# Performance work log

Measured on AMD Instinct MI355X. Metric: run time of the kernel, lower is better.

The kernel has to match this reference:

```python
import jax, jax.numpy as jnp
import numpy as np

DIM = 2048; HEADS = 16; KV_HEADS = 8; HEAD_DIM = 128; RANK = 16; INNER = 5632
B = 2; S = 2048; EPS = 1e-5


def setup_inputs() -> dict:
    key = jax.random.key(0)
    ks = jax.random.split(key, 32)
    r = lambda i, shape, scale=0.02: jax.random.normal(ks[i], shape, jnp.float32) * scale
    theta = jax.random.uniform(ks[0], (S, HEAD_DIM // 2), jnp.float32, 0.0, 2.0 * np.pi)
    return {
        "hidden_states": jax.random.normal(ks[1], (B, S, DIM), jnp.float32),
        "attention_mask": jnp.ones((B, S), jnp.bool_),
        "rope_cos": jnp.cos(theta),
        "rope_sin": jnp.sin(theta),
        "wq_a": r(2, (DIM, RANK), 1.0), "wq_b": r(3, (RANK, DIM)), "bq": r(4, (DIM,)),
        "wk_a": r(5, (DIM, RANK), 1.0), "wk_b": r(6, (RANK, KV_HEADS * HEAD_DIM)), "bk": r(7, (KV_HEADS * HEAD_DIM,)),
        "wv_a": r(8, (DIM, RANK), 1.0), "wv_b": r(9, (RANK, KV_HEADS * HEAD_DIM)), "bv": r(10, (KV_HEADS * HEAD_DIM,)),
        "norm_q_w": 1.0 + r(11, (DIM,)), "norm_q_b": r(12, (DIM,)),
        "norm_k_w": 1.0 + r(13, (KV_HEADS * HEAD_DIM,)), "norm_k_b": r(14, (KV_HEADS * HEAD_DIM,)),
        "w1_a": r(15, (DIM, RANK), 1.0), "w1_b": r(16, (RANK, INNER)), "b1": r(17, (INNER,)),
        "w3_a": r(18, (DIM, RANK), 1.0), "w3_b": r(19, (RANK, INNER)), "b3": r(20, (INNER,)),
        "w2_a": r(21, (INNER, RANK), 1.0), "w2_b": r(22, (RANK, DIM)), "b2": r(23, (DIM,)),
        "norm_w": 1.0 + r(24, (DIM,)), "ffn_norm_w": 1.0 + r(25, (DIM,)),
    }


def _rms(x, w):
    return x * jax.lax.rsqrt(jnp.mean(x * x, axis=-1, keepdims=True) + EPS) * w


def _ln(x, w, b):
    m = jnp.mean(x, axis=-1, keepdims=True)
    v = jnp.mean((x - m) ** 2, axis=-1, keepdims=True)
    return (x - m) * jax.lax.rsqrt(v + EPS) * w + b


def _lora(x, wa, wb, b):
    # faithful to x @ (WA@WB)/rank + b, computed as chained low-rank matmuls
    return (x @ wa) @ wb * (1.0 / RANK) + b


def _rope(x, cos, sin):
    # x: [B,S,H,D]; interleaved-pair complex rotation (diffusers use_real=False)
    x0, x1 = x[..., 0::2], x[..., 1::2]
    c = cos[None, :, None, :]
    s = sin[None, :, None, :]
    return jnp.stack([x0 * c - x1 * s, x0 * s + x1 * c], axis=-1).reshape(x.shape)


def reference(hidden_states, attention_mask, rope_cos, rope_sin,
              wq_a, wq_b, bq, wk_a, wk_b, bk, wv_a, wv_b, bv,
              norm_q_w, norm_q_b, norm_k_w, norm_k_b,
              w1_a, w1_b, b1, w3_a, w3_b, b3, w2_a, w2_b, b2,
              norm_w, ffn_norm_w):
    B_, S_, D_ = hidden_states.shape
    residual = hidden_states
    nh = _rms(hidden_states, norm_w)
    # QKV via LoRA linears; QK layer-norm across heads (before head split)
    q = _ln(_lora(nh, wq_a, wq_b, bq), norm_q_w, norm_q_b)
    k = _ln(_lora(nh, wk_a, wk_b, bk), norm_k_w, norm_k_b)
    v = _lora(nh, wv_a, wv_b, bv)
    q = _rope(q.reshape(B_, S_, HEADS, HEAD_DIM), rope_cos, rope_sin)
    k = _rope(k.reshape(B_, S_, KV_HEADS, HEAD_DIM), rope_cos, rope_sin)
    v = v.reshape(B_, S_, KV_HEADS, HEAD_DIM)
    # GQA: repeat each kv head n_rep times consecutively
    n_rep = HEADS // KV_HEADS
    k = jnp.repeat(k, n_rep, axis=2)
    v = jnp.repeat(v, n_rep, axis=2)
    scale = 1.0 / np.sqrt(HEAD_DIM).astype(np.float32)
    scores = jnp.einsum('bqhd,bkhd->bhqk', q, k) * scale
    neg = jnp.asarray(jnp.finfo(scores.dtype).min, scores.dtype)
    scores = jnp.where(attention_mask[:, None, None, :], scores, neg)
    attn = jax.nn.softmax(scores, axis=-1)
    attn_out = jnp.einsum('bhqk,bkhd->bqhd', attn, v).reshape(B_, S_, D_)
    h = residual + attn_out  # processor output flattened; no to_out in this block
    nf = _rms(h, ffn_norm_w)
    mlp = _lora(jax.nn.silu(_lora(nf, w1_a, w1_b, b1)) * _lora(nf, w3_a, w3_b, b3), w2_a, w2_b, b2)
    return h + mlp
```

## Files before the change

### kernel.cpp

```cpp
#include <hip/hip_runtime.h>
#include <math.h>

typedef unsigned short u16;
typedef unsigned int u32;
typedef __bf16 bf16x8 __attribute__((ext_vector_type(8)));
typedef __bf16 bf16x4 __attribute__((ext_vector_type(4)));
typedef float f32x4 __attribute__((ext_vector_type(4)));

#define DIM 2048
#define NHEADS 16
#define NKVH 8
#define HD 128
#define RANK 16
#define INNER 5632
#define BB 2
#define SS 2048
#define NROWS (BB*SS)
#define EPS 1e-5f
#define QSC2 0.12751743560829201f
#define LOG2E 1.4426950408889634f

__device__ inline float bf2f(u16 u){ u32 x = ((u32)u)<<16; float f; __builtin_memcpy(&f,&x,4); return f; }
__device__ inline u16 f2bf(float f){ u32 u; __builtin_memcpy(&u,&f,4); u32 r = u + 0x7fffu + ((u>>16)&1u); return (u16)(r>>16); }
__device__ inline u32 pack2(float a, float b){ return (u32)f2bf(a) | ((u32)f2bf(b)<<16); }
__device__ inline u16 bfu(float f){ __bf16 b = (__bf16)f; u16 r; __builtin_memcpy(&r,&b,2); return r; }

__device__ inline float blockReduceSum(float v){
  __shared__ float r[4];
  #pragma unroll
  for(int o=1;o<64;o<<=1) v += __shfl_xor(v, o);
  int wv = threadIdx.x>>6;
  __syncthreads();
  if((threadIdx.x&63)==0) r[wv] = v;
  __syncthreads();
  return r[0]+r[1]+r[2]+r[3];
}

__device__ inline f32x4 blockReduceSum4(f32x4 v){
  __shared__ f32x4 r4[4];
  #pragma unroll
  for(int o=1;o<64;o<<=1){
    v.x += __shfl_xor(v.x,o); v.y += __shfl_xor(v.y,o);
    v.z += __shfl_xor(v.z,o); v.w += __shfl_xor(v.w,o);
  }
  int wv = threadIdx.x>>6;
  __syncthreads();
  if((threadIdx.x&63)==0) r4[wv]=v;
  __syncthreads();
  return r4[0]+r4[1]+r4[2]+r4[3];
}

__global__ __launch_bounds__(256) void k_castw(const float* __restrict__ wqb,
                                               const float* __restrict__ wkb,
                                               const float* __restrict__ wvb,
                                               const float* __restrict__ w2b,
                                               u16* __restrict__ wqP,
                                               u16* __restrict__ wkvP,
                                               u16* __restrict__ w2P){
  int bid = blockIdx.x;
  const float* src; u16* dst; int off;
  if(bid<16){ src=wqb; dst=wqP; off=bid; }
  else if(bid<24){ src=wkb; dst=wkvP; off=bid-16; }
  else if(bid<32){ src=wvb; dst=wkvP+16384; off=bid-24; }
  else { src=w2b; dst=w2P; off=bid-32; }
  int base = off*2048 + threadIdx.x*8;
  float4 a = ((const float4*)src)[base/4];
  float4 c = ((const float4*)src)[base/4+1];
  uint4 st;
  st.x = pack2(a.x,a.y); st.y = pack2(a.z,a.w);
  st.z = pack2(c.x,c.y); st.w = pack2(c.z,c.w);
  *(uint4*)&dst[base] = st;
}

__global__ __launch_bounds__(256) void k_rms(const float* __restrict__ x,
                                             const float* __restrict__ w,
                                             u16* __restrict__ out){
  size_t base = (size_t)blockIdx.x*DIM;
  int tid = threadIdx.x;
  float4 v0 = ((const float4*)(x+base))[tid*2];
  float4 v1 = ((const float4*)(x+base))[tid*2+1];
  float ss = v0.x*v0.x+v0.y*v0.y+v0.z*v0.z+v0.w*v0.w
           + v1.x*v1.x+v1.y*v1.y+v1.z*v1.z+v1.w*v1.w;
  ss = blockReduceSum(ss);
  float rstd = rsqrtf(ss*(1.0f/DIM) + EPS);
  float4 w0 = ((const float4*)w)[tid*2];
  float4 w1 = ((const float4*)w)[tid*2+1];
  uint4 st;
  st.x = pack2(v0.x*w0.x*rstd, v0.y*w0.y*rstd);
  st.y = pack2(v0.z*w0.z*rstd, v0.w*w0.w*rstd);
  st.z = pack2(v1.x*w1.x*rstd, v1.y*w1.y*rstd);
  st.w = pack2(v1.z*w1.z*rstd, v1.w*w1.w*rstd);
  *(uint4*)&out[base + tid*8] = st;
}

template<int NMAT>
__global__ __launch_bounds__(256) void k_loraAm(const u16* __restrict__ X,
                                                const float* __restrict__ A0,
                                                const float* __restrict__ A1,
                                                const float* __restrict__ A2,
                                                float* __restrict__ out){
  constexpr int LDO = NMAT*16;
  int mat = blockIdx.x >> 6;
  int blk = blockIdx.x & 63;
  const float* A = (mat==0) ? A0 : ((NMAT>2 && mat==2) ? A2 : A1);
  int tid = threadIdx.x;
  int ks = tid&15, rg = tid>>4;
  int row0 = blk*64 + rg*4;
  float acc[4][16];
  #pragma unroll
  for(int r=0;r<4;r++)
    #pragma unroll
    for(int c=0;c<16;c++) acc[r][c]=0.f;
  const u16* xp = X + (size_t)row0*DIM + ks*128;
  for(int i8=0;i8<16;i8++){
    bf16x8 x0 = *(const bf16x8*)(xp + i8*8);
    bf16x8 x1 = *(const bf16x8*)(xp + DIM + i8*8);
    bf16x8 x2 = *(const bf16x8*)(xp + 2*DIM + i8*8);
    bf16x8 x3 = *(const bf16x8*)(xp + 3*DIM + i8*8);
    #pragma unroll
    for(int e=0;e<8;e++){
      const float4* a = (const float4*)(A + ((size_t)(ks*128 + i8*8 + e))*16);
      float4 a0=a[0], a1=a[1], a2=a[2], a3=a[3];
      float xs0=(float)x0[e], xs1=(float)x1[e], xs2=(float)x2[e], xs3=(float)x3[e];
      #define FMAROW(r, xs) \
        acc[r][0]=fmaf(xs,a0.x,acc[r][0]); acc[r][1]=fmaf(xs,a0.y,acc[r][1]); \
        acc[r][2]=fmaf(xs,a0.z,acc[r][2]); acc[r][3]=fmaf(xs,a0.w,acc[r][3]); \
        acc[r][4]=fmaf(xs,a1.x,acc[r][4]); acc[r][5]=fmaf(xs,a1.y,acc[r][5]); \
        acc[r][6]=fmaf(xs,a1.z,acc[r][6]); acc[r][7]=fmaf(xs,a1.w,acc[r][7]); \
        acc[r][8]=fmaf(xs,a2.x,acc[r][8]); acc[r][9]=fmaf(xs,a2.y,acc[r][9]); \
        acc[r][10]=fmaf(xs,a2.z,acc[r][10]); acc[r][11]=fmaf(xs,a2.w,acc[r][11]); \
        acc[r][12]=fmaf(xs,a3.x,acc[r][12]); acc[r][13]=fmaf(xs,a3.y,acc[r][13]); \
        acc[r][14]=fmaf(xs,a3.z,acc[r][14]); acc[r][15]=fmaf(xs,a3.w,acc[r][15]);
      FMAROW(0, xs0) FMAROW(1, xs1) FMAROW(2, xs2) FMAROW(3, xs3)
      #undef FMAROW
    }
  }
  #pragma unroll
  for(int o=1;o<16;o<<=1){
    #pragma unroll
    for(int r=0;r<4;r++)
      #pragma unroll
      for(int c=0;c<16;c++) acc[r][c] += __shfl_xor(acc[r][c], o);
  }
  if(ks==0){
    #pragma unroll
    for(int r=0;r<4;r++){
      float4* op = (float4*)(out + (size_t)(row0+r)*LDO + mat*16);
      op[0] = make_float4(acc[r][0],acc[r][1],acc[r][2],acc[r][3]);
      op[1] = make_float4(acc[r][4],acc[r][5],acc[r][6],acc[r][7]);
      op[2] = make_float4(acc[r][8],acc[r][9],acc[r][10],acc[r][11]);
      op[3] = make_float4(acc[r][12],acc[r][13],acc[r][14],acc[r][15]);
    }
  }
}

__global__ __launch_bounds__(256) void k_qb(const float* __restrict__ xa,
                                            const u16* __restrict__ wqP,
                                            const float* __restrict__ bq,
                                            const float* __restrict__ nqw,
                                            const float* __restrict__ nqb,
                                            const float* __restrict__ cosT,
                                            const float* __restrict__ sinT,
                                            u16* __restrict__ qout){
  __shared__ u16 wl[16*2048];
  int tid = threadIdx.x;
  #pragma unroll
  for(int ii=0;ii<16;ii++)
    ((uint4*)wl)[tid + 256*ii] = ((const uint4*)wqP)[tid + 256*ii];
  __syncthreads();
  int j0 = tid*8;
  float bqv[8], nwv[8], nbv[8];
  #pragma unroll
  for(int e=0;e<8;e++){ bqv[e]=bq[j0+e]; nwv[e]=nqw[j0+e]; nbv[e]=nqb[j0+e]; }
  int i0 = (j0&127)>>1;
  for(int rp=0;rp<4;rp++){
    int row = blockIdx.x*8 + rp*2;
    float pre[2][8];
    #pragma unroll
    for(int rr=0;rr<2;rr++){
      float xq[16];
      #pragma unroll
      for(int r=0;r<16;r++) xq[r] = xa[(size_t)(row+rr)*48 + r];
      #pragma unroll
      for(int e=0;e<8;e++) pre[rr][e]=0.f;
      #pragma unroll
      for(int r=0;r<16;r++){
        bf16x8 wv = *(const bf16x8*)&wl[r*2048 + j0];
        #pragma unroll
        for(int e=0;e<8;e++) pre[rr][e] = fmaf(xq[r], (float)wv[e], pre[rr][e]);
      }
      #pragma unroll
      for(int e=0;e<8;e++) pre[rr][e] = pre[rr][e]*0.0625f + bqv[e];
    }
    f32x4 sv = (f32x4){0.f,0.f,0.f,0.f};
    #pragma unroll
    for(int e=0;e<8;e++){
      sv.x += pre[0][e]; sv.y += pre[0][e]*pre[0][e];
      sv.z += pre[1][e]; sv.w += pre[1][e]*pre[1][e];
    }
    f32x4 red = blockReduceSum4(sv);
    #pragma unroll
    for(int rr=0;rr<2;rr++){
      float mu  = (rr?red.z:red.x)*(1.0f/DIM);
      float var = (rr?red.w:red.y)*(1.0f/DIM) - mu*mu;
      float rstd = rsqrtf(var + EPS);
      float qn[8];
      #pragma unroll
      for(int e=0;e<8;e++) qn[e] = (pre[rr][e]-mu)*rstd*nwv[e] + nbv[e];
      int spos = (row+rr) & (SS-1);
      const float* cp = cosT + spos*64;
      const float* sp = sinT + spos*64;
      uint4 st;
      u32 pk[4];
      #pragma unroll
      for(int p=0;p<4;p++){
        float c = cp[i0+p], sn = sp[i0+p];
        float x0 = qn[2*p], x1 = qn[2*p+1];
        pk[p] = pack2((x0*c - x1*sn)*QSC2, (x0*sn + x1*c)*QSC2);
      }
      st.x=pk[0]; st.y=pk[1]; st.z=pk[2]; st.w=pk[3];
      *(uint4*)&qout[(size_t)(row+rr)*2048 + j0] = st;
    }
  }
}

__global__ __launch_bounds__(256) void k_kvb(const float* __restrict__ xa,
                                             const u16* __restrict__ wkvP,
                                             const float* __restrict__ bk,
                                             const float* __restrict__ nkw,
                                             const float* __restrict__ nkb,
                                             const float* __restrict__ bv,
                                             const float* __restrict__ cosT,
                                             const float* __restrict__ sinT,
                                             u16* __restrict__ kout,
                                             u16* __restrict__ vout){
  __shared__ u16 wl[2*16*1024];
  int tid = threadIdx.x;
  #pragma unroll
  for(int ii=0;ii<16;ii++)
    ((uint4*)wl)[tid + 256*ii] = ((const uint4*)wkvP)[tid + 256*ii];
  __syncthreads();
  int j0 = tid*4;
  float bkv[4], nwv[4], nbv[4], bvv[4];
  #pragma unroll
  for(int e=0;e<4;e++){ bkv[e]=bk[j0+e]; nwv[e]=nkw[j0+e]; nbv[e]=nkb[j0+e]; bvv[e]=bv[j0+e]; }
  int i0 = (j0&127)>>1;
  for(int rp=0;rp<4;rp++){
    int row = blockIdx.x*8 + rp*2;
    float pk_[2][4], pv_[2][4];
    #pragma unroll
    for(int rr=0;rr<2;rr++){
      float xk[16], xv[16];
      #pragma unroll
      for(int r=0;r<16;r++){ xk[r]=xa[(size_t)(row+rr)*48+16+r]; xv[r]=xa[(size_t)(row+rr)*48+32+r]; }
      #pragma unroll
      for(int e=0;e<4;e++){ pk_[rr][e]=0.f; pv_[rr][e]=0.f; }
      #pragma unroll
      for(int r=0;r<16;r++){
        bf16x4 wk4 = *(const bf16x4*)&wl[r*1024 + j0];
        bf16x4 wv4 = *(const bf16x4*)&wl[16384 + r*1024 + j0];
        #pragma unroll
        for(int e=0;e<4;e++){ pk_[rr][e]=fmaf(xk[r],(float)wk4[e],pk_[rr][e]); pv_[rr][e]=fmaf(xv[r],(float)wv4[e],pv_[rr][e]); }
      }
      #pragma unroll
      for(int e=0;e<4;e++){ pk_[rr][e]=pk_[rr][e]*0.0625f + bkv[e]; pv_[rr][e]=pv_[rr][e]*0.0625f + bvv[e]; }
    }
    f32x4 sv = (f32x4){0.f,0.f,0.f,0.f};
    #pragma unroll
    for(int e=0;e<4;e++){
      sv.x += pk_[0][e]; sv.y += pk_[0][e]*pk_[0][e];
      sv.z += pk_[1][e]; sv.w += pk_[1][e]*pk_[1][e];
    }
    f32x4 red = blockReduceSum4(sv);
    #pragma unroll
    for(int rr=0;rr<2;rr++){
      float mu  = (rr?red.z:red.x)*(1.0f/1024.0f);
      float var = (rr?red.w:red.y)*(1.0f/1024.0f) - mu*mu;
      float rstd = rsqrtf(var + EPS);
      float kn[4];
      #pragma unroll
      for(int e=0;e<4;e++) kn[e] = (pk_[rr][e]-mu)*rstd*nwv[e] + nbv[e];
      int spos = (row+rr) & (SS-1);
      const float* cp = cosT + spos*64;
      const float* sp = sinT + spos*64;
      uint2 stk;
      { float c=cp[i0],   sn=sp[i0];   stk.x = pack2(kn[0]*c - kn[1]*sn, kn[0]*sn + kn[1]*c); }
      { float c=cp[i0+1], sn=sp[i0+1]; stk.y = pack2(kn[2]*c - kn[3]*sn, kn[2]*sn + kn[3]*c); }
      *(uint2*)&kout[(size_t)(row+rr)*1024 + j0] = stk;
      uint2 stv; stv.x = pack2(pv_[rr][0],pv_[rr][1]); stv.y = pack2(pv_[rr][2],pv_[rr][3]);
      *(uint2*)&vout[(size_t)(row+rr)*1024 + j0] = stv;
    }
  }
}

__global__ __launch_bounds__(256) void k_vt(const u16* __restrict__ v,
                                            u16* __restrict__ vt){
  __shared__ u16 tl[64*68];
  int bid = blockIdx.x;
  int st = bid & 31;
  int dt = (bid>>5) & 1;
  int bh = bid>>6;
  int b = bh>>3, kvh = bh&7;
  int tid = threadIdx.x;
  int s0 = st*64, d0 = dt*64;
  {
    int s_l = tid>>2, dg = tid&3;
    const u16* src = v + ((size_t)(b*SS + s0 + s_l)*NKVH + kvh)*HD + d0 + dg*16;
    *(uint4*)&tl[s_l*68 + dg*16]     = *(const uint4*)(src);
    *(uint4*)&tl[s_l*68 + dg*16 + 8] = *(const uint4*)(src + 8);
  }
  __syncthreads();
  {
    int d_l = tid>>2, sg = tid&3;
    u32 pk[8];
    #pragma unroll
    for(int i=0;i<8;i++){
      u16 a = tl[(sg*16 + 2*i)*68 + d_l];
      u16 c = tl[(sg*16 + 2*i+1)*68 + d_l];
      pk[i] = (u32)a | ((u32)c<<16);
    }
    u16* dst = vt + ((size_t)bh*HD + d0 + d_l)*SS + s0 + sg*16;
    ((uint4*)dst)[0] = make_uint4(pk[0],pk[1],pk[2],pk[3]);
    ((uint4*)dst)[1] = make_uint4(pk[4],pk[5],pk[6],pk[7]);
  }
}

__global__ __launch_bounds__(256,2) void k_attn(const u16* __restrict__ qb,
                                                const u16* __restrict__ kb,
                                                const u16* __restrict__ vt,
                                                const float* __restrict__ resid,
                                                float* __restrict__ out){
  __shared__ u16 Kc[16*520];
  __shared__ u16 Vc[8*1032];
  __shared__ u16 Pl[4][32*72];
  int bid = ((int)blockIdx.x & 7)*64 + ((int)blockIdx.x >> 3);
  int qt = bid & 15;
  int h  = (bid>>4) & 15;
  int b  = bid>>8;
  int kvh = h>>1;
  int tid = threadIdx.x;
  int w = tid>>6, lane = tid&63;
  int l16 = lane&15, lg = lane>>4;

  bf16x8 qa[2][4];
  #pragma unroll
  for(int m=0;m<2;m++){
    const u16* qp = qb + ((size_t)(b*SS + qt*128 + w*32 + m*16 + l16))*DIM + h*HD + lg*8;
    #pragma unroll
    for(int c=0;c<4;c++) qa[m][c] = *(const bf16x8*)(qp + c*32);
  }
  f32x4 acc[2][8];
  #pragma unroll
  for(int m=0;m<2;m++)
    #pragma unroll
    for(int n=0;n<8;n++) acc[m][n] = (f32x4){0.f,0.f,0.f,0.f};
  f32x4 lacc0 = (f32x4){0.f,0.f,0.f,0.f};
  f32x4 lacc1 = (f32x4){0.f,0.f,0.f,0.f};
  bf16x8 ones;
  #pragma unroll
  for(int e=0;e<8;e++) ones[e] = (__bf16)1.0f;

  u16* Pw = Pl[w];
  const u16* vtb = vt + (size_t)(b*NKVH + kvh)*HD*SS;
  const u16* kbb = kb + ((size_t)(b*SS)*NKVH + kvh)*HD;
  int k_key = tid>>4, k_dg = tid&15;
  int v_d   = tid>>3, v_kc = tid&7;
  uint4 kA,kB,kC,kD,vA,vB,vC,vD;

#define LOAD_STAGE(KT) do{ \
    const u16* ksrc_ = kbb + (size_t)(KT)*64*1024; \
    const u16* vsrc_ = vtb + (KT)*64; \
    kA = *(const uint4*)(ksrc_ + (size_t)(k_key     )*1024 + k_dg*8); \
    kB = *(const uint4*)(ksrc_ + (size_t)(k_key + 16)*1024 + k_dg*8); \
    kC = *(const uint4*)(ksrc_ + (size_t)(k_key + 32)*1024 + k_dg*8); \
    kD = *(const uint4*)(ksrc_ + (size_t)(k_key + 48)*1024 + k_dg*8); \
    vA = *(const uint4*)(vsrc_ + (size_t)(v_d      )*SS + v_kc*8); \
    vB = *(const uint4*)(vsrc_ + (size_t)(v_d + 32 )*SS + v_kc*8); \
    vC = *(const uint4*)(vsrc_ + (size_t)(v_d + 64 )*SS + v_kc*8); \
    vD = *(const uint4*)(vsrc_ + (size_t)(v_d + 96 )*SS + v_kc*8); \
  }while(0)
#define STORE_STAGE() do{ \
    *(uint4*)&Kc[k_dg*520 + (k_key     )*8] = kA; \
    *(uint4*)&Kc[k_dg*520 + (k_key + 16)*8] = kB; \
    *(uint4*)&Kc[k_dg*520 + (k_key + 32)*8] = kC; \
    *(uint4*)&Kc[k_dg*520 + (k_key + 48)*8] = kD; \
    *(uint4*)&Vc[v_kc*1032 + (v_d      )*8] = vA; \
    *(uint4*)&Vc[v_kc*1032 + (v_d + 32 )*8] = vB; \
    *(uint4*)&Vc[v_kc*1032 + (v_d + 64 )*8] = vC; \
    *(uint4*)&Vc[v_kc*1032 + (v_d + 96 )*8] = vD; \
  }while(0)

  LOAD_STAGE(0);
  STORE_STAGE();
  __syncthreads();

  for(int kt=0; kt<SS/64; kt++){
    bool more = (kt+1) < SS/64;
    if(more) LOAD_STAGE(kt+1);
    #pragma unroll
    for(int nb=0;nb<4;nb++){
      f32x4 s0 = (f32x4){0.f,0.f,0.f,0.f};
      f32x4 s1 = (f32x4){0.f,0.f,0.f,0.f};
      #pragma unroll
      for(int c=0;c<4;c++){
        bf16x8 kf = *(const bf16x8*)&Kc[(c*4+lg)*520 + (nb*16+l16)*8];
        s0 = __builtin_amdgcn_mfma_f32_16x16x32_bf16(qa[0][c], kf, s0, 0,0,0);
        s1 = __builtin_amdgcn_mfma_f32_16x16x32_bf16(qa[1][c], kf, s1, 0,0,0);
      }
      #pragma unroll
      for(int r=0;r<4;r++){
        Pw[(lg*4+r)*72 + nb*16 + l16]      = bfu(exp2f(s0[r]));
        Pw[(16+lg*4+r)*72 + nb*16 + l16]   = bfu(exp2f(s1[r]));
      }
    }
    #pragma unroll
    for(int ks=0;ks<2;ks++){
      bf16x8 pa0 = *(const bf16x8*)&Pw[l16*72 + ks*32 + lg*8];
      bf16x8 pa1 = *(const bf16x8*)&Pw[(16+l16)*72 + ks*32 + lg*8];
      lacc0 = __builtin_amdgcn_mfma_f32_16x16x32_bf16(pa0, ones, lacc0, 0,0,0);
      lacc1 = __builtin_amdgcn_mfma_f32_16x16x32_bf16(pa1, ones, lacc1, 0,0,0);
      #pragma unroll
      for(int n=0;n<8;n++){
        bf16x8 vf = *(const bf16x8*)&Vc[(ks*4+lg)*1032 + (n*16+l16)*8];
        acc[0][n] = __builtin_amdgcn_mfma_f32_16x16x32_bf16(pa0, vf, acc[0][n], 0,0,0);
        acc[1][n] = __builtin_amdgcn_mfma_f32_16x16x32_bf16(pa1, vf, acc[1][n], 0,0,0);
      }
    }
    __syncthreads();
    if(more) STORE_STAGE();
    __syncthreads();
  }
#undef LOAD_STAGE
#undef STORE_STAGE
  #pragma unroll
  for(int m=0;m<2;m++){
    #pragma unroll
    for(int r=0;r<4;r++){
      float lv = m ? lacc1[r] : lacc0[r];
      float inv = __builtin_amdgcn_rcpf(lv);
      int row = qt*128 + w*32 + m*16 + lg*4 + r;
      size_t base = ((size_t)(b*SS + row))*DIM + h*HD;
      #pragma unroll
      for(int n=0;n<8;n++){
        int d = n*16 + l16;
        out[base + d] = resid[base + d] + acc[m][n][r]*inv;
      }
    }
  }
}

__global__ __launch_bounds__(256) void k_pack(const float* __restrict__ w1b,
                                              const float* __restrict__ w3b,
                                              const float* __restrict__ w2a,
                                              u16* __restrict__ wpk){
  int j = blockIdx.x*256 + threadIdx.x;
  u32 pw[24];
  #pragma unroll
  for(int i=0;i<8;i++) pw[i]    = pack2(w1b[(size_t)(2*i)*INNER+j], w1b[(size_t)(2*i+1)*INNER+j]);
  #pragma unroll
  for(int i=0;i<8;i++) pw[8+i]  = pack2(w3b[(size_t)(2*i)*INNER+j], w3b[(size_t)(2*i+1)*INNER+j]);
  const float4* wp = (const float4*)(w2a + (size_t)j*16);
  #pragma unroll
  for(int q=0;q<4;q++){ float4 t=wp[q];
    pw[16+2*q] = pack2(t.x,t.y); pw[17+2*q] = pack2(t.z,t.w); }
  uint4* dst = (uint4*)(wpk + (size_t)j*48);
  #pragma unroll
  for(int i=0;i<6;i++) dst[i] = make_uint4(pw[4*i],pw[4*i+1],pw[4*i+2],pw[4*i+3]);
}

__global__ __launch_bounds__(256,1) void k_ffn(const float* __restrict__ t13,
                                               const u16* __restrict__ wpk,
                                               const float* __restrict__ b1,
                                               const float* __restrict__ b3,
                                               float* __restrict__ racc){
  __shared__ float tl[4][32];
  __shared__ float red[4][64];
  int tid = threadIdx.x;
  int row0 = blockIdx.x*4;
  if(tid<128) tl[tid>>5][tid&31] = t13[(size_t)row0*32 + tid];
  __syncthreads();
  float acc[64];
  #pragma unroll
  for(int v=0;v<64;v++) acc[v]=0.f;
  for(int ii=0;ii<INNER/256;ii++){
    int j = tid + 256*ii;
    const u16* wr = wpk + (size_t)j*48;
    bf16x8 W1a = *(const bf16x8*)(wr),    bf16x8_W1b_ = *(const bf16x8*)(wr+8);
    bf16x8 W1b = bf16x8_W1b_;
    bf16x8 W3a = *(const bf16x8*)(wr+16), W3b = *(const bf16x8*)(wr+24);
    bf16x8 W2a = *(const bf16x8*)(wr+32), W2b = *(const bf16x8*)(wr+40);
    float bb1 = b1[j], bb3 = b3[j];
    #pragma unroll
    for(int rr=0;rr<4;rr++){
      float a1=0.f, a3=0.f;
      #pragma unroll
      for(int r=0;r<8;r++){
        a1 = fmaf(tl[rr][r],    (float)W1a[r], a1);
        a1 = fmaf(tl[rr][8+r],  (float)W1b[r], a1);
        a3 = fmaf(tl[rr][16+r], (float)W3a[r], a3);
        a3 = fmaf(tl[rr][24+r], (float)W3b[r], a3);
      }
      a1 = a1*0.0625f + bb1;
      a3 = a3*0.0625f + bb3;
      float u = a1*__builtin_amdgcn_rcpf(1.0f+exp2f(-a1*LOG2E)) * a3;
      #pragma unroll
      for(int c=0;c<8;c++){
        acc[rr*16+c]   = fmaf(u, (float)W2a[c], acc[rr*16+c]);
        acc[rr*16+8+c] = fmaf(u, (float)W2b[c], acc[rr*16+8+c]);
      }
    }
  }
  #pragma unroll
  for(int o=1;o<64;o<<=1){
    #pragma unroll
    for(int v=0;v<64;v++) acc[v] += __shfl_xor(acc[v], o);
  }
  int wv = tid>>6, lane = tid&63;
  if(lane==0){
    #pragma unroll
    for(int v=0;v<64;v++) red[wv][v] = acc[v];
  }
  __syncthreads();
  if(tid<64){
    float sum = red[0][tid]+red[1][tid]+red[2][tid]+red[3][tid];
    racc[(size_t)(row0 + (tid>>4))*16 + (tid&15)] = sum;
  }
}

__global__ __launch_bounds__(256) void k_out(const float* __restrict__ racc,
                                             const u16* __restrict__ w2P,
                                             const float* __restrict__ b2,
                                             float* __restrict__ io){
  __shared__ u16 wl[16*2048];
  int tid = threadIdx.x;
  #pragma unroll
  for(int ii=0;ii<16;ii++)
    ((uint4*)wl)[tid + 256*ii] = ((const uint4*)w2P)[tid + 256*ii];
  __syncthreads();
  int j0 = tid*8;
  float b2v[8];
  #pragma unroll
  for(int e=0;e<8;e++) b2v[e] = b2[j0+e];
  for(int rr=0;rr<8;rr++){
    int row = blockIdx.x*8 + rr;
    float rc[16];
    #pragma unroll
    for(int r=0;r<16;r++) rc[r] = racc[(size_t)row*16 + r];
    float pre[8];
    #pragma unroll
    for(int e=0;e<8;e++) pre[e]=0.f;
    #pragma unroll
    for(int r=0;r<16;r++){
      bf16x8 wv = *(const bf16x8*)&wl[r*2048 + j0];
      #pragma unroll
      for(int e=0;e<8;e++) pre[e] = fmaf(rc[r], (float)wv[e], pre[e]);
    }
    float* op = io + (size_t)row*DIM + j0;
    float4 h0 = ((const float4*)op)[0];
    float4 h1 = ((const float4*)op)[1];
    float4 o0, o1;
    o0.x = h0.x + pre[0]*0.0625f + b2v[0];
    o0.y = h0.y + pre[1]*0.0625f + b2v[1];
    o0.z = h0.z + pre[2]*0.0625f + b2v[2];
    o0.w = h0.w + pre[3]*0.0625f + b2v[3];
    o1.x = h1.x + pre[4]*0.0625f + b2v[4];
    o1.y = h1.y + pre[5]*0.0625f + b2v[5];
    o1.z = h1.z + pre[6]*0.0625f + b2v[6];
    o1.w = h1.w + pre[7]*0.0625f + b2v[7];
    ((float4*)op)[0] = o0;
    ((float4*)op)[1] = o1;
  }
}

extern "C" void kernel_launch(void* const* d_in, const int* in_sizes, int n_in,
                              void* d_out, int out_size, void* d_ws, size_t ws_size,
                              hipStream_t stream){
  const float* hidden = (const float*)d_in[0];
  const float* cosT = (const float*)d_in[2];
  const float* sinT = (const float*)d_in[3];
  const float* wq_a = (const float*)d_in[4];
  const float* wq_b = (const float*)d_in[5];
  const float* bq   = (const float*)d_in[6];
  const float* wk_a = (const float*)d_in[7];
  const float* wk_b = (const float*)d_in[8];
  const float* bk   = (const float*)d_in[9];
  const float* wv_a = (const float*)d_in[10];
  const float* wv_b = (const float*)d_in[11];
  const float* bv   = (const float*)d_in[12];
  const float* nqw  = (const float*)d_in[13];
  const float* nqb  = (const float*)d_in[14];
  const float* nkw  = (const float*)d_in[15];
  const float* nkb  = (const float*)d_in[16];
  const float* w1a  = (const float*)d_in[17];
  const float* w1b  = (const float*)d_in[18];
  const float* b1   = (const float*)d_in[19];
  const float* w3a  = (const float*)d_in[20];
  const float* w3b  = (const float*)d_in[21];
  const float* b3   = (const float*)d_in[22];
  const float* w2a  = (const float*)d_in[23];
  const float* w2b  = (const float*)d_in[24];
  const float* b2   = (const float*)d_in[25];
  const float* normw  = (const float*)d_in[26];
  const float* fnormw = (const float*)d_in[27];
  float* out = (float*)d_out;

  char* p = (char*)d_ws;
  u16* bufA = (u16*)p; p += (size_t)NROWS*DIM*2;
  u16* qbuf = (u16*)p; p += (size_t)NROWS*DIM*2;
  u16* kbuf = (u16*)p; p += (size_t)NROWS*1024*2;
  u16* vbuf = (u16*)p; p += (size_t)NROWS*1024*2;
  float* xa   = (float*)p; p += (size_t)NROWS*48*4;
  float* t13  = (float*)p; p += (size_t)NROWS*32*4;
  float* racc = (float*)p; p += (size_t)NROWS*16*4;
  u16* wpk  = (u16*)p; p += (size_t)INNER*48*2;
  u16* wqP  = (u16*)p; p += (size_t)16*2048*2;
  u16* wkvP = (u16*)p; p += (size_t)2*16*1024*2;
  u16* w2P  = (u16*)p; p += (size_t)16*2048*2;
  u16* vtbuf = bufA;

  k_castw<<<48,256,0,stream>>>(wq_b, wk_b, wv_b, w2b, wqP, wkvP, w2P);
  k_pack<<<INNER/256,256,0,stream>>>(w1b, w3b, w2a, wpk);
  k_rms<<<NROWS,256,0,stream>>>(hidden, normw, bufA);
  k_loraAm<3><<<192,256,0,stream>>>(bufA, wq_a, wk_a, wv_a, xa);
  k_qb <<<NROWS/8,256,0,stream>>>(xa, wqP, bq, nqw, nqb, cosT, sinT, qbuf);
  k_kvb<<<NROWS/8,256,0,stream>>>(xa, wkvP, bk, nkw, nkb, bv, cosT, sinT, kbuf, vbuf);
  k_vt<<<1024,256,0,stream>>>(vbuf, vtbuf);
  k_attn<<<512,256,0,stream>>>(qbuf, kbuf, vtbuf, hidden, out);
  k_rms<<<NROWS,256,0,stream>>>(out, fnormw, bufA);
  k_loraAm<2><<<128,256,0,stream>>>(bufA, w1a, w3a, nullptr, t13);
  k_ffn<<<NROWS/4,256,0,stream>>>(t13, wpk, b1, b3, racc);
  k_out<<<NROWS/8,256,0,stream>>>(racc, w2P, b2, out);
}
```

Before: 389.9 us.

## Fuse RMSNorm into the LoRA-A projection, reading fp32 activations directly

Removes the separate RMSNorm kernels and the bf16 normalized intermediate buffer. Each row's sum of squares is now computed inside the LoRA-A kernel by a 16-lane shuffle reduction, and the fp32 input is normalized on the fly. Rows per block drop from 64 to 16 (one row per 16-thread group) and the grid grows. In exchange, each fp32 row is read twice and once per A matrix, so 3x or 2x redundant activation reads, and register reuse of the A weights across rows is lost.

Result: slower. 568.3 us (+45.7%).

```diff
diff --git a/kernel.cpp b/kernel.cpp
--- a/kernel.cpp
+++ b/kernel.cpp
@@ -24,17 +24,6 @@
 __device__ inline u16 f2bf(float f){ u32 u; __builtin_memcpy(&u,&f,4); u32 r = u + 0x7fffu + ((u>>16)&1u); return (u16)(r>>16); }
 __device__ inline u32 pack2(float a, float b){ return (u32)f2bf(a) | ((u32)f2bf(b)<<16); }
 __device__ inline u16 bfu(float f){ __bf16 b = (__bf16)f; u16 r; __builtin_memcpy(&r,&b,2); return r; }
-
-__device__ inline float blockReduceSum(float v){
-  __shared__ float r[4];
-  #pragma unroll
-  for(int o=1;o<64;o<<=1) v += __shfl_xor(v, o);
-  int wv = threadIdx.x>>6;
-  __syncthreads();
-  if((threadIdx.x&63)==0) r[wv] = v;
-  __syncthreads();
-  return r[0]+r[1]+r[2]+r[3];
-}
 
 __device__ inline f32x4 blockReduceSum4(f32x4 v){
   __shared__ f32x4 r4[4];
@@ -72,85 +61,66 @@
   *(uint4*)&dst[base] = st;
 }
 
-__global__ __launch_bounds__(256) void k_rms(const float* __restrict__ x,
-                                             const float* __restrict__ w,
-                                             u16* __restrict__ out){
-  size_t base = (size_t)blockIdx.x*DIM;
-  int tid = threadIdx.x;
-  float4 v0 = ((const float4*)(x+base))[tid*2];
-  float4 v1 = ((const float4*)(x+base))[tid*2+1];
-  float ss = v0.x*v0.x+v0.y*v0.y+v0.z*v0.z+v0.w*v0.w
-           + v1.x*v1.x+v1.y*v1.y+v1.z*v1.z+v1.w*v1.w;
-  ss = blockReduceSum(ss);
-  float rstd = rsqrtf(ss*(1.0f/DIM) + EPS);
-  float4 w0 = ((const float4*)w)[tid*2];
-  float4 w1 = ((const float4*)w)[tid*2+1];
-  uint4 st;
-  st.x = pack2(v0.x*w0.x*rstd, v0.y*w0.y*rstd);
-  st.y = pack2(v0.z*w0.z*rstd, v0.w*w0.w*rstd);
-  st.z = pack2(v1.x*w1.x*rstd, v1.y*w1.y*rstd);
-  st.w = pack2(v1.z*w1.z*rstd, v1.w*w1.w*rstd);
-  *(uint4*)&out[base + tid*8] = st;
-}
-
 template<int NMAT>
-__global__ __launch_bounds__(256) void k_loraAm(const u16* __restrict__ X,
-                                                const float* __restrict__ A0,
-                                                const float* __restrict__ A1,
-                                                const float* __restrict__ A2,
-                                                float* __restrict__ out){
+__global__ __launch_bounds__(256) void k_loraF(const float* __restrict__ X,
+                                               const float* __restrict__ nw,
+                                               const float* __restrict__ A0,
+                                               const float* __restrict__ A1,
+                                               const float* __restrict__ A2,
+                                               float* __restrict__ out){
   constexpr int LDO = NMAT*16;
-  int mat = blockIdx.x >> 6;
-  int blk = blockIdx.x & 63;
+  int mat = blockIdx.x >> 8;
+  int blk = blockIdx.x & 255;
   const float* A = (mat==0) ? A0 : ((NMAT>2 && mat==2) ? A2 : A1);
   int tid = threadIdx.x;
   int ks = tid&15, rg = tid>>4;
-  int row0 = blk*64 + rg*4;
-  float acc[4][16];
-  #pragma unroll
-  for(int r=0;r<4;r++)
-    #pragma unroll
-    for(int c=0;c<16;c++) acc[r][c]=0.f;
-  const u16* xp = X + (size_t)row0*DIM + ks*128;
-  for(int i8=0;i8<16;i8++){
-    bf16x8 x0 = *(const bf16x8*)(xp + i8*8);
-    bf16x8 x1 = *(const bf16x8*)(xp + DIM + i8*8);
-    bf16x8 x2 = *(const bf16x8*)(xp + 2*DIM + i8*8);
-    bf16x8 x3 = *(const bf16x8*)(xp + 3*DIM + i8*8);
-    #pragma unroll
-    for(int e=0;e<8;e++){
-      const float4* a = (const float4*)(A + ((size_t)(ks*128 + i8*8 + e))*16);
+  int row = blk*16 + rg;
+  const float* xp = X + (size_t)row*DIM + ks*128;
+  const float* wp = nw + ks*128;
+  float ss = 0.f;
+  #pragma unroll
+  for(int i=0;i<32;i++){
+    float4 v = ((const float4*)xp)[i];
+    ss += v.x*v.x + v.y*v.y + v.z*v.z + v.w*v.w;
+  }
+  ss += __shfl_xor(ss,1); ss += __shfl_xor(ss,2);
+  ss += __shfl_xor(ss,4); ss += __shfl_xor(ss,8);
+  float rstd = rsqrtf(ss*(1.0f/DIM) + EPS);
+  float acc[16];
+  #pragma unroll
+  for(int c=0;c<16;c++) acc[c]=0.f;
+  for(int i4=0;i4<32;i4++){
+    float4 xv = ((const float4*)xp)[i4];
+    float4 wv = ((const float4*)wp)[i4];
+    float xn[4];
+    xn[0]=xv.x*wv.x*rstd; xn[1]=xv.y*wv.y*rstd;
+    xn[2]=xv.z*wv.z*rstd; xn[3]=xv.w*wv.w*rstd;
+    #pragma unroll
+    for(int j=0;j<4;j++){
+      const float4* a = (const float4*)(A + ((size_t)(ks*128 + i4*4 + j))*16);
       float4 a0=a[0], a1=a[1], a2=a[2], a3=a[3];
-      float xs0=(float)x0[e], xs1=(float)x1[e], xs2=(float)x2[e], xs3=(float)x3[e];
-      #define FMAROW(r, xs) \
-        acc[r][0]=fmaf(xs,a0.x,acc[r][0]); acc[r][1]=fmaf(xs,a0.y,acc[r][1]); \
-        acc[r][2]=fmaf(xs,a0.z,acc[r][2]); acc[r][3]=fmaf(xs,a0.w,acc[r][3]); \
-        acc[r][4]=fmaf(xs,a1.x,acc[r][4]); acc[r][5]=fmaf(xs,a1.y,acc[r][5]); \
-        acc[r][6]=fmaf(xs,a1.z,acc[r][6]); acc[r][7]=fmaf(xs,a1.w,acc[r][7]); \
-        acc[r][8]=fmaf(xs,a2.x,acc[r][8]); acc[r][9]=fmaf(xs,a2.y,acc[r][9]); \
-        acc[r][10]=fmaf(xs,a2.z,acc[r][10]); acc[r][11]=fmaf(xs,a2.w,acc[r][11]); \
-        acc[r][12]=fmaf(xs,a3.x,acc[r][12]); acc[r][13]=fmaf(xs,a3.y,acc[r][13]); \
-        acc[r][14]=fmaf(xs,a3.z,acc[r][14]); acc[r][15]=fmaf(xs,a3.w,acc[r][15]);
-      FMAROW(0, xs0) FMAROW(1, xs1) FMAROW(2, xs2) FMAROW(3, xs3)
-      #undef FMAROW
+      float xs = xn[j];
+      acc[0]=fmaf(xs,a0.x,acc[0]);  acc[1]=fmaf(xs,a0.y,acc[1]);
+      acc[2]=fmaf(xs,a0.z,acc[2]);  acc[3]=fmaf(xs,a0.w,acc[3]);
+      acc[4]=fmaf(xs,a1.x,acc[4]);  acc[5]=fmaf(xs,a1.y,acc[5]);
+      acc[6]=fmaf(xs,a1.z,acc[6]);  acc[7]=fmaf(xs,a1.w,acc[7]);
+      acc[8]=fmaf(xs,a2.x,acc[8]);  acc[9]=fmaf(xs,a2.y,acc[9]);
+      acc[10]=fmaf(xs,a2.z,acc[10]); acc[11]=fmaf(xs,a2.w,acc[11]);
+      acc[12]=fmaf(xs,a3.x,acc[12]); acc[13]=fmaf(xs,a3.y,acc[13]);
+      acc[14]=fmaf(xs,a3.z,acc[14]); acc[15]=fmaf(xs,a3.w,acc[15]);
     }
   }
   #pragma unroll
   for(int o=1;o<16;o<<=1){
     #pragma unroll
-    for(int r=0;r<4;r++)
-      #pragma unroll
-      for(int c=0;c<16;c++) acc[r][c] += __shfl_xor(acc[r][c], o);
+    for(int c=0;c<16;c++) acc[c] += __shfl_xor(acc[c], o);
   }
   if(ks==0){
-    #pragma unroll
-    for(int r=0;r<4;r++){
-      float4* op = (float4*)(out + (size_t)(row0+r)*LDO + mat*16);
-      op[0] = make_float4(acc[r][0],acc[r][1],acc[r][2],acc[r][3]);
-      op[1] = make_float4(acc[r][4],acc[r][5],acc[r][6],acc[r][7]);
-      op[2] = make_float4(acc[r][8],acc[r][9],acc[r][10],acc[r][11]);
-      op[3] = make_float4(acc[r][12],acc[r][13],acc[r][14],acc[r][15]);
-    }
+    float4* op = (float4*)(out + (size_t)row*LDO + mat*16);
+    op[0] = make_float4(acc[0],acc[1],acc[2],acc[3]);
+    op[1] = make_float4(acc[4],acc[5],acc[6],acc[7]);
+    op[2] = make_float4(acc[8],acc[9],acc[10],acc[11]);
+    op[3] = make_float4(acc[12],acc[13],acc[14],acc[15]);
   }
 }
 
@@ -485,10 +455,12 @@
   for(int ii=0;ii<INNER/256;ii++){
     int j = tid + 256*ii;
     const u16* wr = wpk + (size_t)j*48;
-    bf16x8 W1a = *(const bf16x8*)(wr),    bf16x8_W1b_ = *(const bf16x8*)(wr+8);
-    bf16x8 W1b = bf16x8_W1b_;
-    bf16x8 W3a = *(const bf16x8*)(wr+16), W3b = *(const bf16x8*)(wr+24);
-    bf16x8 W2a = *(const bf16x8*)(wr+32), W2b = *(const bf16x8*)(wr+40);
+    bf16x8 W1a = *(const bf16x8*)(wr);
+    bf16x8 W1b = *(const bf16x8*)(wr+8);
+    bf16x8 W3a = *(const bf16x8*)(wr+16);
+    bf16x8 W3b = *(const bf16x8*)(wr+24);
+    bf16x8 W2a = *(const bf16x8*)(wr+32);
+    bf16x8 W2b = *(const bf16x8*)(wr+40);
     float bb1 = b1[j], bb3 = b3[j];
     #pragma unroll
     for(int rr=0;rr<4;rr++){
@@ -620,14 +592,12 @@
 
   k_castw<<<48,256,0,stream>>>(wq_b, wk_b, wv_b, w2b, wqP, wkvP, w2P);
   k_pack<<<INNER/256,256,0,stream>>>(w1b, w3b, w2a, wpk);
-  k_rms<<<NROWS,256,0,stream>>>(hidden, normw, bufA);
-  k_loraAm<3><<<192,256,0,stream>>>(bufA, wq_a, wk_a, wv_a, xa);
+  k_loraF<3><<<768,256,0,stream>>>(hidden, normw, wq_a, wk_a, wv_a, xa);
   k_qb <<<NROWS/8,256,0,stream>>>(xa, wqP, bq, nqw, nqb, cosT, sinT, qbuf);
   k_kvb<<<NROWS/8,256,0,stream>>>(xa, wkvP, bk, nkw, nkb, bv, cosT, sinT, kbuf, vbuf);
   k_vt<<<1024,256,0,stream>>>(vbuf, vtbuf);
   k_attn<<<512,256,0,stream>>>(qbuf, kbuf, vtbuf, hidden, out);
-  k_rms<<<NROWS,256,0,stream>>>(out, fnormw, bufA);
-  k_loraAm<2><<<128,256,0,stream>>>(bufA, w1a, w3a, nullptr, t13);
+  k_loraF<2><<<512,256,0,stream>>>(out, fnormw, w1a, w3a, nullptr, t13);
   k_ffn<<<NROWS/4,256,0,stream>>>(t13, wpk, b1, b3, racc);
   k_out<<<NROWS/8,256,0,stream>>>(racc, w2P, b2, out);
 }
```

## Split LoRA down-projection over K into four chunks with separate reduction kernel

Applied to the files above, without the earlier changes.

The rank-16 down-projection kernel is split along the reduction dimension into four K-chunks, which raises the grid from 192/128 blocks to 768/512 so the 256-CU GPU is better occupied. Each block writes partial sums to a new workspace buffer, and a small reduction kernel adds the four partials into the existing xa/t13 buffers. In exchange it adds an extra launch and extra partial-sum global traffic. The k_ffn weight-load edit is cosmetic.

Result: faster. 344.0 us (-11.8%).

```diff
diff --git a/kernel.cpp b/kernel.cpp
--- a/kernel.cpp
+++ b/kernel.cpp
@@ -94,14 +94,17 @@
 }
 
 template<int NMAT>
-__global__ __launch_bounds__(256) void k_loraAm(const u16* __restrict__ X,
+__global__ __launch_bounds__(256) void k_loraAs(const u16* __restrict__ X,
                                                 const float* __restrict__ A0,
                                                 const float* __restrict__ A1,
                                                 const float* __restrict__ A2,
-                                                float* __restrict__ out){
+                                                float* __restrict__ part){
   constexpr int LDO = NMAT*16;
-  int mat = blockIdx.x >> 6;
-  int blk = blockIdx.x & 63;
+  int bid = blockIdx.x;
+  int mat = bid >> 8;
+  int rem = bid & 255;
+  int kc  = rem & 3;
+  int blk = rem >> 2;
   const float* A = (mat==0) ? A0 : ((NMAT>2 && mat==2) ? A2 : A1);
   int tid = threadIdx.x;
   int ks = tid&15, rg = tid>>4;
@@ -111,15 +114,17 @@
   for(int r=0;r<4;r++)
     #pragma unroll
     for(int c=0;c<16;c++) acc[r][c]=0.f;
-  const u16* xp = X + (size_t)row0*DIM + ks*128;
-  for(int i8=0;i8<16;i8++){
+  const u16* xp = X + (size_t)row0*DIM + kc*512 + ks*32;
+  #pragma unroll
+  for(int i8=0;i8<4;i8++){
     bf16x8 x0 = *(const bf16x8*)(xp + i8*8);
     bf16x8 x1 = *(const bf16x8*)(xp + DIM + i8*8);
     bf16x8 x2 = *(const bf16x8*)(xp + 2*DIM + i8*8);
     bf16x8 x3 = *(const bf16x8*)(xp + 3*DIM + i8*8);
     #pragma unroll
     for(int e=0;e<8;e++){
-      const float4* a = (const float4*)(A + ((size_t)(ks*128 + i8*8 + e))*16);
+      int k = kc*512 + ks*32 + i8*8 + e;
+      const float4* a = (const float4*)(A + (size_t)k*16);
       float4 a0=a[0], a1=a[1], a2=a[2], a3=a[3];
       float xs0=(float)x0[e], xs1=(float)x1[e], xs2=(float)x2[e], xs3=(float)x3[e];
       #define FMAROW(r, xs) \
@@ -145,13 +150,23 @@
   if(ks==0){
     #pragma unroll
     for(int r=0;r<4;r++){
-      float4* op = (float4*)(out + (size_t)(row0+r)*LDO + mat*16);
+      float4* op = (float4*)(part + ((size_t)kc*NROWS + row0+r)*LDO + mat*16);
       op[0] = make_float4(acc[r][0],acc[r][1],acc[r][2],acc[r][3]);
       op[1] = make_float4(acc[r][4],acc[r][5],acc[r][6],acc[r][7]);
       op[2] = make_float4(acc[r][8],acc[r][9],acc[r][10],acc[r][11]);
       op[3] = make_float4(acc[r][12],acc[r][13],acc[r][14],acc[r][15]);
     }
   }
+}
+
+__global__ __launch_bounds__(256) void k_lred(const float* __restrict__ part,
+                                              float* __restrict__ out, int n4){
+  int i = blockIdx.x*256 + threadIdx.x;
+  if(i >= n4) return;
+  const float4* p = (const float4*)part;
+  float4 a = p[i], b = p[i+n4], c = p[i+2*n4], d = p[i+3*n4];
+  ((float4*)out)[i] = make_float4(a.x+b.x+c.x+d.x, a.y+b.y+c.y+d.y,
+                                  a.z+b.z+c.z+d.z, a.w+b.w+c.w+d.w);
 }
 
 __global__ __launch_bounds__(256) void k_qb(const float* __restrict__ xa,
@@ -485,10 +500,12 @@
   for(int ii=0;ii<INNER/256;ii++){
     int j = tid + 256*ii;
     const u16* wr = wpk + (size_t)j*48;
-    bf16x8 W1a = *(const bf16x8*)(wr),    bf16x8_W1b_ = *(const bf16x8*)(wr+8);
-    bf16x8 W1b = bf16x8_W1b_;
-    bf16x8 W3a = *(const bf16x8*)(wr+16), W3b = *(const bf16x8*)(wr+24);
-    bf16x8 W2a = *(const bf16x8*)(wr+32), W2b = *(const bf16x8*)(wr+40);
+    bf16x8 W1a = *(const bf16x8*)(wr);
+    bf16x8 W1b = *(const bf16x8*)(wr+8);
+    bf16x8 W3a = *(const bf16x8*)(wr+16);
+    bf16x8 W3b = *(const bf16x8*)(wr+24);
+    bf16x8 W2a = *(const bf16x8*)(wr+32);
+    bf16x8 W2b = *(const bf16x8*)(wr+40);
     float bb1 = b1[j], bb3 = b3[j];
     #pragma unroll
     for(int rr=0;rr<4;rr++){
@@ -616,18 +633,21 @@
   u16* wqP  = (u16*)p; p += (size_t)16*2048*2;
   u16* wkvP = (u16*)p; p += (size_t)2*16*1024*2;
   u16* w2P  = (u16*)p; p += (size_t)16*2048*2;
+  float* part = (float*)p; p += (size_t)4*NROWS*48*4;
   u16* vtbuf = bufA;
 
   k_castw<<<48,256,0,stream>>>(wq_b, wk_b, wv_b, w2b, wqP, wkvP, w2P);
   k_pack<<<INNER/256,256,0,stream>>>(w1b, w3b, w2a, wpk);
   k_rms<<<NROWS,256,0,stream>>>(hidden, normw, bufA);
-  k_loraAm<3><<<192,256,0,stream>>>(bufA, wq_a, wk_a, wv_a, xa);
+  k_loraAs<3><<<768,256,0,stream>>>(bufA, wq_a, wk_a, wv_a, part);
+  k_lred<<<192,256,0,stream>>>(part, xa, NROWS*48/4);
   k_qb <<<NROWS/8,256,0,stream>>>(xa, wqP, bq, nqw, nqb, cosT, sinT, qbuf);
   k_kvb<<<NROWS/8,256,0,stream>>>(xa, wkvP, bk, nkw, nkb, bv, cosT, sinT, kbuf, vbuf);
   k_vt<<<1024,256,0,stream>>>(vbuf, vtbuf);
   k_attn<<<512,256,0,stream>>>(qbuf, kbuf, vtbuf, hidden, out);
   k_rms<<<NROWS,256,0,stream>>>(out, fnormw, bufA);
-  k_loraAm<2><<<128,256,0,stream>>>(bufA, w1a, w3a, nullptr, t13);
+  k_loraAs<2><<<512,256,0,stream>>>(bufA, w1a, w3a, nullptr, part);
+  k_lred<<<128,256,0,stream>>>(part, t13, NROWS*32/4);
   k_ffn<<<NROWS/4,256,0,stream>>>(t13, wpk, b1, b3, racc);
   k_out<<<NROWS/8,256,0,stream>>>(racc, w2P, b2, out);
 }
```
